# Performance work log

Hardware: AMD Instinct MI355X
Metric: run time of the kernel (lower is better)

The kernel has to match this reference:

```python
import jax, jax.numpy as jnp
import numpy as np

N = 100000        # nodes
E_RAND = 1600000  # random edges (avg degree 16)
D_IN = 64
D_OUT = 64


def setup_inputs() -> dict:
    key = jax.random.key(0)
    k1, k2, k3, k4, k5 = jax.random.split(key, 5)
    x = jax.random.normal(k1, (N, D_IN), dtype=jnp.float32)
    rows = jax.random.randint(k2, (E_RAND,), 0, N)
    cols = jax.random.randint(k3, (E_RAND,), 0, N)
    loops = jnp.arange(N)  # self loops appended at the end (matches remove+add_self_loops order)
    edge_index = jnp.stack([jnp.concatenate([rows, loops]),
                            jnp.concatenate([cols, loops])]).astype(jnp.int64)
    W = (jax.random.normal(k4, (D_IN, D_OUT), dtype=jnp.float32) / np.float32(np.sqrt(D_IN)))
    b = jax.random.normal(k5, (D_OUT,), dtype=jnp.float32) * 0.01
    return {"x": x, "edge_index": edge_index, "W": W, "b": b}


def reference(x, edge_index, W, b):
    row, col = edge_index[0], edge_index[1]
    # lin(x[row]) == (x @ W + b)[row]; transform once then gather (cheaper, same math)
    xl = x @ W + b                      # [N, D_OUT]
    x_i = xl[row]                       # [E, D_OUT] gather by destination
    x_j = xl[col]                       # [E, D_OUT] gather by source
    alpha = jnp.sum(x_i * x_j, axis=-1)  # [E] per-edge score
    alpha = jax.nn.leaky_relu(alpha, negative_slope=0.2)
    # segment-wise softmax over neighborhoods keyed by row
    m = jax.ops.segment_max(alpha, row, num_segments=N)
    m = jnp.where(jnp.isfinite(m), m, 0.0)   # isolated nodes -> -inf max, neutralize
    e = jnp.exp(alpha - m[row])
    s = jax.ops.segment_sum(e, row, num_segments=N)
    alpha = e / (s[row] + 1e-16)
    # dropout(p=0.6) skipped: reference runs in eval mode (deterministic)
    out = jax.ops.segment_sum(x_j * alpha[:, None], row, num_segments=N)  # [N, D_OUT]
    return out
```

## Files before the change

### kernel.cpp

```cpp
#include <hip/hip_runtime.h>
#include <hip/hip_bf16.h>


#define LEAKY_SLOPE 0.2f
#define BK_SHIFT 6
#define BK_NODES 64
#define CAP 1408
#define NBMAX 2048
#define CH 8192

typedef __attribute__((ext_vector_type(8))) short short8;
typedef __attribute__((ext_vector_type(4))) float f32x4;

struct HiLo { short hi, lo; };

__device__ __forceinline__ HiLo split2(float f) {
    HiLo r;
    unsigned u = __float_as_uint(f);
    r.hi = (short)(u >> 16);
    float fh = __uint_as_float(u & 0xFFFF0000u);
    r.lo = (short)(__float_as_uint(f - fh) >> 16);
    return r;
}

__device__ __forceinline__ float bfbits2f(unsigned short u) {
    return __uint_as_float(((unsigned)u) << 16);
}

__global__ __launch_bounds__(256) void k_linear(const float* __restrict__ x,
                                                const float* __restrict__ W,
                                                const float* __restrict__ b,
                                                float* __restrict__ xl,
                                                unsigned short* __restrict__ xlh,
                                                int* __restrict__ cursor,
                                                int ncur, int N, int ntiles) {
    __shared__ __align__(16) short Wt_hi[64 * 72];
    __shared__ __align__(16) short Wt_lo[64 * 72];

    int tid = threadIdx.x;
    int gid = blockIdx.x * 256 + tid;
    if (gid < ncur) cursor[gid] = 0;

    for (int i = tid; i < 4096; i += 256) {
        int k = i >> 6, n = i & 63;
        HiLo h = split2(W[i]);
        Wt_hi[n * 72 + k] = h.hi;
        Wt_lo[n * 72 + k] = h.lo;
    }
    __syncthreads();

    int wave = tid >> 6, lane = tid & 63;
    int tile = blockIdx.x * 4 + wave;
    if (tile >= ntiles) return;
    int node0 = tile * 16;

    int m = lane & 15;
    int quad = lane >> 4;

    f32x4 acc[4] = {{0.f, 0.f, 0.f, 0.f}, {0.f, 0.f, 0.f, 0.f},
                    {0.f, 0.f, 0.f, 0.f}, {0.f, 0.f, 0.f, 0.f}};

#pragma unroll
    for (int ks = 0; ks < 64; ks += 32) {
        const float* xr = x + (size_t)(node0 + m) * 64 + ks + quad * 8;
        float4 xa = *(const float4*)xr;
        float4 xb = *(const float4*)(xr + 4);
        short8 a_hi, a_lo;
        {
            HiLo h0 = split2(xa.x), h1 = split2(xa.y), h2 = split2(xa.z), h3 = split2(xa.w);
            HiLo h4 = split2(xb.x), h5 = split2(xb.y), h6 = split2(xb.z), h7 = split2(xb.w);
            a_hi[0] = h0.hi; a_lo[0] = h0.lo;  a_hi[1] = h1.hi; a_lo[1] = h1.lo;
            a_hi[2] = h2.hi; a_lo[2] = h2.lo;  a_hi[3] = h3.hi; a_lo[3] = h3.lo;
            a_hi[4] = h4.hi; a_lo[4] = h4.lo;  a_hi[5] = h5.hi; a_lo[5] = h5.lo;
            a_hi[6] = h6.hi; a_lo[6] = h6.lo;  a_hi[7] = h7.hi; a_lo[7] = h7.lo;
        }

#pragma unroll
        for (int g = 0; g < 4; ++g) {
            int n = g * 16 + m;
            int off = n * 72 + ks + quad * 8;
            short8 bh = *(const short8*)&Wt_hi[off];
            short8 bl = *(const short8*)&Wt_lo[off];
            acc[g] = __builtin_amdgcn_mfma_f32_16x16x32_bf16(a_hi, bh, acc[g], 0, 0, 0);
            acc[g] = __builtin_amdgcn_mfma_f32_16x16x32_bf16(a_lo, bh, acc[g], 0, 0, 0);
            acc[g] = __builtin_amdgcn_mfma_f32_16x16x32_bf16(a_hi, bl, acc[g], 0, 0, 0);
        }
    }

#pragma unroll
    for (int g = 0; g < 4; ++g) {
        float bias = b[g * 16 + m];
#pragma unroll
        for (int r = 0; r < 4; ++r) {
            int node = node0 + quad * 4 + r;
            if (node < N) {
                float v = acc[g][r] + bias;
                xl[(size_t)node * 64 + g * 16 + m] = v;
                xlh[(size_t)node * 64 + g * 16 + m] =
                    (unsigned short)(__float_as_uint(v) >> 16);
            }
        }
    }
}

__global__ __launch_bounds__(1024) void k_msplit(const int* __restrict__ row,
                                                 const int* __restrict__ col,
                                                 int* __restrict__ cursor,
                                                 unsigned* __restrict__ staging,
                                                 int E, int NB) {
    __shared__ int cnt[NBMAX], base[NBMAX], pos[NBMAX];
    int tid = threadIdx.x;
    int e0 = blockIdx.x * CH;
    int e1 = min(E, e0 + CH);

    for (int i = tid; i < NB; i += 1024) { cnt[i] = 0; pos[i] = 0; }
    __syncthreads();
    for (int e = e0 + tid; e < e1; e += 1024)
        atomicAdd(&cnt[row[e] >> BK_SHIFT], 1);
    __syncthreads();
    for (int i = tid; i < NB; i += 1024)
        base[i] = cnt[i] ? atomicAdd(&cursor[i * 16], cnt[i]) : 0;
    __syncthreads();
    for (int e = e0 + tid; e < e1; e += 1024) {
        int r = row[e], c = col[e];
        int bkt = r >> BK_SHIFT;
        int p = base[bkt] + atomicAdd(&pos[bkt], 1);
        if (p < CAP)
            staging[(size_t)bkt * CAP + p] =
                ((unsigned)(r & (BK_NODES - 1)) << 17) | (unsigned)c;
    }
}

__device__ __forceinline__ float red16(float d) {
    d += __shfl_xor(d, 1, 64);
    d += __shfl_xor(d, 2, 64);
    d += __shfl_xor(d, 4, 64);
    d += __shfl_xor(d, 8, 64);
    return d;
}

__device__ __forceinline__ void upd(float& m, float& l, float4& acc,
                                    float a, float4 xj) {
    if (a <= m) {
        float p = __expf(a - m);
        l += p;
        acc.x += p * xj.x; acc.y += p * xj.y;
        acc.z += p * xj.z; acc.w += p * xj.w;
    } else {
        float sc = __expf(m - a);
        l = l * sc + 1.0f;
        acc.x = acc.x * sc + xj.x; acc.y = acc.y * sc + xj.y;
        acc.z = acc.z * sc + xj.z; acc.w = acc.w * sc + xj.w;
        m = a;
    }
}

__device__ __forceinline__ float4 ld_bf4(const unsigned short* p) {
    ushort4 u = *(const ushort4*)p;
    float4 f;
    f.x = bfbits2f(u.x); f.y = bfbits2f(u.y);
    f.z = bfbits2f(u.z); f.w = bfbits2f(u.w);
    return f;
}

__global__ __launch_bounds__(256) void k_sortfused(const float* __restrict__ xl,
                                                   const unsigned short* __restrict__ xlh,
                                                   const unsigned* __restrict__ staging,
                                                   const int* __restrict__ cursor,
                                                   float* __restrict__ out, int N) {
    __shared__ int colsh[CAP];
    __shared__ int deg[BK_NODES], sc[BK_NODES], cur[BK_NODES];

    int bkt = blockIdx.x;
    int tid = threadIdx.x;
    int cnt = min(cursor[bkt * 16], CAP);
    const unsigned* st = staging + (size_t)bkt * CAP;

    if (tid < BK_NODES) { deg[tid] = 0; cur[tid] = 0; }
    __syncthreads();

    for (int e = tid; e < cnt; e += 256) atomicAdd(&deg[st[e] >> 17], 1);
    __syncthreads();

    if (tid < BK_NODES) sc[tid] = deg[tid];
    __syncthreads();
#pragma unroll
    for (int o = 1; o < BK_NODES; o <<= 1) {
        int v = 0;
        if (tid < BK_NODES && tid >= o) v = sc[tid - o];
        __syncthreads();
        if (tid < BK_NODES) sc[tid] += v;
        __syncthreads();
    }

    for (int e = tid; e < cnt; e += 256) {
        unsigned pk = st[e];
        int rl = pk >> 17;
        int p = sc[rl] - deg[rl] + atomicAdd(&cur[rl], 1);
        colsh[p] = (int)(pk & 0x1FFFFu);
    }
    __syncthreads();

    int grp = tid >> 4;
    int g = tid & 15;
    for (int n0 = grp; n0 < BK_NODES; n0 += 16) {
        int node = bkt * BK_NODES + n0;
        if (node >= N) continue;
        int beg = sc[n0] - deg[n0];
        int end = sc[n0];
        float4 xi = ((const float4*)xl)[(size_t)node * 16 + g];

        float m = -INFINITY, l = 0.0f;
        float4 acc = {0.f, 0.f, 0.f, 0.f};

        int e = beg;
        for (; e + 4 <= end; e += 4) {
            int c0 = colsh[e], c1 = colsh[e + 1], c2 = colsh[e + 2], c3 = colsh[e + 3];
            float4 xj0 = ld_bf4(xlh + (size_t)c0 * 64 + 4 * g);
            float4 xj1 = ld_bf4(xlh + (size_t)c1 * 64 + 4 * g);
            float4 xj2 = ld_bf4(xlh + (size_t)c2 * 64 + 4 * g);
            float4 xj3 = ld_bf4(xlh + (size_t)c3 * 64 + 4 * g);
            float d0 = red16(xi.x * xj0.x + xi.y * xj0.y + xi.z * xj0.z + xi.w * xj0.w);
            float d1 = red16(xi.x * xj1.x + xi.y * xj1.y + xi.z * xj1.z + xi.w * xj1.w);
            float d2 = red16(xi.x * xj2.x + xi.y * xj2.y + xi.z * xj2.z + xi.w * xj2.w);
            float d3 = red16(xi.x * xj3.x + xi.y * xj3.y + xi.z * xj3.z + xi.w * xj3.w);
            upd(m, l, acc, (d0 >= 0.f) ? d0 : LEAKY_SLOPE * d0, xj0);
            upd(m, l, acc, (d1 >= 0.f) ? d1 : LEAKY_SLOPE * d1, xj1);
            upd(m, l, acc, (d2 >= 0.f) ? d2 : LEAKY_SLOPE * d2, xj2);
            upd(m, l, acc, (d3 >= 0.f) ? d3 : LEAKY_SLOPE * d3, xj3);
        }
        for (; e < end; ++e) {
            int c = colsh[e];
            float4 xj = ld_bf4(xlh + (size_t)c * 64 + 4 * g);
            float d = red16(xi.x * xj.x + xi.y * xj.y + xi.z * xj.z + xi.w * xj.w);
            upd(m, l, acc, (d >= 0.f) ? d : LEAKY_SLOPE * d, xj);
        }
        float inv = 1.0f / (l + 1e-16f);
        float4 o = {acc.x * inv, acc.y * inv, acc.z * inv, acc.w * inv};
        ((float4*)out)[(size_t)node * 16 + g] = o;
    }
}

extern "C" void kernel_launch(void* const* d_in, const int* in_sizes, int n_in,
                              void* d_out, int out_size, void* d_ws, size_t ws_size,
                              hipStream_t stream) {
    const float* x = (const float*)d_in[0];
    const int* ei = (const int*)d_in[1];
    const float* W = (const float*)d_in[2];
    const float* b = (const float*)d_in[3];

    const int N = in_sizes[0] / 64;
    const int E = in_sizes[1] / 2;
    const int NO = N * 64;
    const int NB = (N + BK_NODES - 1) >> BK_SHIFT;
    const int* row = ei;
    const int* col = ei + E;

    float* out = (float*)d_out;

    float* ws = (float*)d_ws;
    float* xl           = ws;
    unsigned short* xlh = (unsigned short*)(xl + (size_t)NO);
    int* cursor         = (int*)(xlh + (size_t)NO);
    unsigned* staging   = (unsigned*)(cursor + NB * 16);

    const int ntiles = (N + 15) / 16;
    const int lblocks = (ntiles + 3) / 4;
    k_linear<<<lblocks, 256, 0, stream>>>(x, W, b, xl, xlh, cursor, NB * 16, N, ntiles);
    k_msplit<<<(E + CH - 1) / CH, 1024, 0, stream>>>(row, col, cursor, staging, E, NB);
    k_sortfused<<<NB, 256, 0, stream>>>(xl, xlh, staging, cursor, out, N);
}
```

Measured before the change: 184.5 us.

## Merge linear and bucket-split into one launch with per-chunk offset tables

Fuses the linear-transform kernel and the edge bucketing kernel into a single launch whose blocks branch on block index, sharing LDS through a union. Global atomics on per-bucket cursors are replaced by per-chunk local prefix scans that write chunk-major staging plus an offset table. The aggregation kernel then rebuilds each bucket's edge list by scanning the per-chunk lengths and binary-searching chunks. This removes one launch and the global atomic contention and cursor zeroing, at the cost of scattered gathers from many chunks in the consumer, 256-thread split blocks instead of 1024, and a 128-chunk limit.

```diff
diff --git a/kernel.cpp b/kernel.cpp
--- a/kernel.cpp
+++ b/kernel.cpp
@@ -6,8 +6,9 @@
 #define BK_SHIFT 6
 #define BK_NODES 64
 #define CAP 1408
-#define NBMAX 2048
-#define CH 8192
+#define NBMAX 1600
+#define CH 16384
+#define NCH_MAX 128
 
 typedef __attribute__((ext_vector_type(8))) short short8;
 typedef __attribute__((ext_vector_type(4))) float f32x4;
@@ -27,107 +28,124 @@
     return __uint_as_float(((unsigned)u) << 16);
 }
 
-__global__ __launch_bounds__(256) void k_linear(const float* __restrict__ x,
-                                                const float* __restrict__ W,
-                                                const float* __restrict__ b,
-                                                float* __restrict__ xl,
-                                                unsigned short* __restrict__ xlh,
-                                                int* __restrict__ cursor,
-                                                int ncur, int N, int ntiles) {
-    __shared__ __align__(16) short Wt_hi[64 * 72];
-    __shared__ __align__(16) short Wt_lo[64 * 72];
-
+union PreShMem {
+    struct { short wt_hi[64 * 72]; short wt_lo[64 * 72]; } lin;
+    struct { int cnt[NBMAX], scn[NBMAX], pos[NBMAX], segsum[256]; } ms;
+};
+
+__global__ __launch_bounds__(256) void k_pre(const float* __restrict__ x,
+                                             const float* __restrict__ W,
+                                             const float* __restrict__ b,
+                                             const int* __restrict__ row,
+                                             const int* __restrict__ col,
+                                             float* __restrict__ xl,
+                                             unsigned short* __restrict__ xlh,
+                                             int* __restrict__ ofs,
+                                             unsigned* __restrict__ staging,
+                                             int N, int E, int NB,
+                                             int ntiles, int lblocks) {
+    __shared__ PreShMem sh;
     int tid = threadIdx.x;
-    int gid = blockIdx.x * 256 + tid;
-    if (gid < ncur) cursor[gid] = 0;
-
-    for (int i = tid; i < 4096; i += 256) {
-        int k = i >> 6, n = i & 63;
-        HiLo h = split2(W[i]);
-        Wt_hi[n * 72 + k] = h.hi;
-        Wt_lo[n * 72 + k] = h.lo;
-    }
-    __syncthreads();
-
-    int wave = tid >> 6, lane = tid & 63;
-    int tile = blockIdx.x * 4 + wave;
-    if (tile >= ntiles) return;
-    int node0 = tile * 16;
-
-    int m = lane & 15;
-    int quad = lane >> 4;
-
-    f32x4 acc[4] = {{0.f, 0.f, 0.f, 0.f}, {0.f, 0.f, 0.f, 0.f},
-                    {0.f, 0.f, 0.f, 0.f}, {0.f, 0.f, 0.f, 0.f}};
-
-#pragma unroll
-    for (int ks = 0; ks < 64; ks += 32) {
-        const float* xr = x + (size_t)(node0 + m) * 64 + ks + quad * 8;
-        float4 xa = *(const float4*)xr;
-        float4 xb = *(const float4*)(xr + 4);
-        short8 a_hi, a_lo;
-        {
-            HiLo h0 = split2(xa.x), h1 = split2(xa.y), h2 = split2(xa.z), h3 = split2(xa.w);
-            HiLo h4 = split2(xb.x), h5 = split2(xb.y), h6 = split2(xb.z), h7 = split2(xb.w);
-            a_hi[0] = h0.hi; a_lo[0] = h0.lo;  a_hi[1] = h1.hi; a_lo[1] = h1.lo;
-            a_hi[2] = h2.hi; a_lo[2] = h2.lo;  a_hi[3] = h3.hi; a_lo[3] = h3.lo;
-            a_hi[4] = h4.hi; a_lo[4] = h4.lo;  a_hi[5] = h5.hi; a_lo[5] = h5.lo;
-            a_hi[6] = h6.hi; a_lo[6] = h6.lo;  a_hi[7] = h7.hi; a_lo[7] = h7.lo;
+
+    if ((int)blockIdx.x < lblocks) {
+        for (int i = tid; i < 4096; i += 256) {
+            int k = i >> 6, n = i & 63;
+            HiLo h = split2(W[i]);
+            sh.lin.wt_hi[n * 72 + k] = h.hi;
+            sh.lin.wt_lo[n * 72 + k] = h.lo;
+        }
+        __syncthreads();
+
+        int wave = tid >> 6, lane = tid & 63;
+        int tile = blockIdx.x * 4 + wave;
+        if (tile >= ntiles) return;
+        int node0 = tile * 16;
+        int m = lane & 15;
+        int quad = lane >> 4;
+
+        f32x4 acc[4] = {{0.f, 0.f, 0.f, 0.f}, {0.f, 0.f, 0.f, 0.f},
+                        {0.f, 0.f, 0.f, 0.f}, {0.f, 0.f, 0.f, 0.f}};
+
+#pragma unroll
+        for (int ks = 0; ks < 64; ks += 32) {
+            const float* xr = x + (size_t)(node0 + m) * 64 + ks + quad * 8;
+            float4 xa = *(const float4*)xr;
+            float4 xb = *(const float4*)(xr + 4);
+            short8 a_hi, a_lo;
+            {
+                HiLo h0 = split2(xa.x), h1 = split2(xa.y), h2 = split2(xa.z), h3 = split2(xa.w);
+                HiLo h4 = split2(xb.x), h5 = split2(xb.y), h6 = split2(xb.z), h7 = split2(xb.w);
+                a_hi[0] = h0.hi; a_lo[0] = h0.lo;  a_hi[1] = h1.hi; a_lo[1] = h1.lo;
+                a_hi[2] = h2.hi; a_lo[2] = h2.lo;  a_hi[3] = h3.hi; a_lo[3] = h3.lo;
+                a_hi[4] = h4.hi; a_lo[4] = h4.lo;  a_hi[5] = h5.hi; a_lo[5] = h5.lo;
+                a_hi[6] = h6.hi; a_lo[6] = h6.lo;  a_hi[7] = h7.hi; a_lo[7] = h7.lo;
+            }
+#pragma unroll
+            for (int g = 0; g < 4; ++g) {
+                int n = g * 16 + m;
+                int off = n * 72 + ks + quad * 8;
+                short8 bh = *(const short8*)&sh.lin.wt_hi[off];
+                short8 bl = *(const short8*)&sh.lin.wt_lo[off];
+                acc[g] = __builtin_amdgcn_mfma_f32_16x16x32_bf16(a_hi, bh, acc[g], 0, 0, 0);
+                acc[g] = __builtin_amdgcn_mfma_f32_16x16x32_bf16(a_lo, bh, acc[g], 0, 0, 0);
+                acc[g] = __builtin_amdgcn_mfma_f32_16x16x32_bf16(a_hi, bl, acc[g], 0, 0, 0);
+            }
         }
 
 #pragma unroll
         for (int g = 0; g < 4; ++g) {
-            int n = g * 16 + m;
-            int off = n * 72 + ks + quad * 8;
-            short8 bh = *(const short8*)&Wt_hi[off];
-            short8 bl = *(const short8*)&Wt_lo[off];
-            acc[g] = __builtin_amdgcn_mfma_f32_16x16x32_bf16(a_hi, bh, acc[g], 0, 0, 0);
-            acc[g] = __builtin_amdgcn_mfma_f32_16x16x32_bf16(a_lo, bh, acc[g], 0, 0, 0);
-            acc[g] = __builtin_amdgcn_mfma_f32_16x16x32_bf16(a_hi, bl, acc[g], 0, 0, 0);
-        }
-    }
-
-#pragma unroll
-    for (int g = 0; g < 4; ++g) {
-        float bias = b[g * 16 + m];
-#pragma unroll
-        for (int r = 0; r < 4; ++r) {
-            int node = node0 + quad * 4 + r;
-            if (node < N) {
-                float v = acc[g][r] + bias;
-                xl[(size_t)node * 64 + g * 16 + m] = v;
-                xlh[(size_t)node * 64 + g * 16 + m] =
-                    (unsigned short)(__float_as_uint(v) >> 16);
+            float bias = b[g * 16 + m];
+#pragma unroll
+            for (int r = 0; r < 4; ++r) {
+                int node = node0 + quad * 4 + r;
+                if (node < N) {
+                    float v = acc[g][r] + bias;
+                    xl[(size_t)node * 64 + g * 16 + m] = v;
+                    xlh[(size_t)node * 64 + g * 16 + m] =
+                        (unsigned short)(__float_as_uint(v) >> 16);
+                }
             }
         }
-    }
-}
-
-__global__ __launch_bounds__(1024) void k_msplit(const int* __restrict__ row,
-                                                 const int* __restrict__ col,
-                                                 int* __restrict__ cursor,
-                                                 unsigned* __restrict__ staging,
-                                                 int E, int NB) {
-    __shared__ int cnt[NBMAX], base[NBMAX], pos[NBMAX];
-    int tid = threadIdx.x;
-    int e0 = blockIdx.x * CH;
-    int e1 = min(E, e0 + CH);
-
-    for (int i = tid; i < NB; i += 1024) { cnt[i] = 0; pos[i] = 0; }
-    __syncthreads();
-    for (int e = e0 + tid; e < e1; e += 1024)
-        atomicAdd(&cnt[row[e] >> BK_SHIFT], 1);
-    __syncthreads();
-    for (int i = tid; i < NB; i += 1024)
-        base[i] = cnt[i] ? atomicAdd(&cursor[i * 16], cnt[i]) : 0;
-    __syncthreads();
-    for (int e = e0 + tid; e < e1; e += 1024) {
-        int r = row[e], c = col[e];
-        int bkt = r >> BK_SHIFT;
-        int p = base[bkt] + atomicAdd(&pos[bkt], 1);
-        if (p < CAP)
-            staging[(size_t)bkt * CAP + p] =
-                ((unsigned)(r & (BK_NODES - 1)) << 17) | (unsigned)c;
+    } else {
+        int vbk = (int)blockIdx.x - lblocks;
+        int e0 = vbk * CH;
+        int e1 = min(E, e0 + CH);
+
+        for (int i = tid; i < NB; i += 256) { sh.ms.cnt[i] = 0; sh.ms.pos[i] = 0; }
+        __syncthreads();
+
+        for (int e = e0 + tid; e < e1; e += 256)
+            atomicAdd(&sh.ms.cnt[row[e] >> BK_SHIFT], 1);
+        __syncthreads();
+
+        const int SEG = (NBMAX + 255) / 256;
+        int segbeg = tid * SEG;
+        int segend = min(NB, segbeg + SEG);
+        int s = 0;
+        for (int i = segbeg; i < segend; ++i) { int v = sh.ms.cnt[i]; sh.ms.scn[i] = s; s += v; }
+        sh.ms.segsum[tid] = s;
+        __syncthreads();
+        for (int o = 1; o < 256; o <<= 1) {
+            int v = (tid >= o) ? sh.ms.segsum[tid - o] : 0;
+            __syncthreads();
+            sh.ms.segsum[tid] += v;
+            __syncthreads();
+        }
+        int segoff = (tid == 0) ? 0 : sh.ms.segsum[tid - 1];
+        for (int i = segbeg; i < segend; ++i) sh.ms.scn[i] += segoff;
+        __syncthreads();
+
+        int* orow = ofs + (size_t)vbk * (NB + 1);
+        for (int i = tid; i < NB; i += 256) orow[i] = sh.ms.scn[i];
+        if (tid == 0) orow[NB] = e1 - e0;
+
+        unsigned* stg = staging + (size_t)vbk * CH;
+        for (int e = e0 + tid; e < e1; e += 256) {
+            int r = row[e], c = col[e];
+            int bkt = r >> BK_SHIFT;
+            int p = sh.ms.scn[bkt] + atomicAdd(&sh.ms.pos[bkt], 1);
+            stg[p] = ((unsigned)(r & (BK_NODES - 1)) << 17) | (unsigned)c;
+        }
     }
 }
 
@@ -163,23 +181,62 @@
     return f;
 }
 
+__device__ __forceinline__ float dot4(float4 a, float4 b) {
+    return a.x * b.x + a.y * b.y + a.z * b.z + a.w * b.w;
+}
+
 __global__ __launch_bounds__(256) void k_sortfused(const float* __restrict__ xl,
                                                    const unsigned short* __restrict__ xlh,
                                                    const unsigned* __restrict__ staging,
-                                                   const int* __restrict__ cursor,
-                                                   float* __restrict__ out, int N) {
+                                                   const int* __restrict__ ofs,
+                                                   float* __restrict__ out,
+                                                   int N, int NB, int nch) {
+    __shared__ int raw[CAP];
     __shared__ int colsh[CAP];
     __shared__ int deg[BK_NODES], sc[BK_NODES], cur[BK_NODES];
+    __shared__ int lenarr[NCH_MAX];
+    __shared__ int chbeg[NCH_MAX + 1];
+    __shared__ int chofs[NCH_MAX];
 
     int bkt = blockIdx.x;
     int tid = threadIdx.x;
-    int cnt = min(cursor[bkt * 16], CAP);
-    const unsigned* st = staging + (size_t)bkt * CAP;
+
+    if (tid < NCH_MAX) {
+        int len = 0;
+        if (tid < nch) {
+            const int* orow = ofs + (size_t)tid * (NB + 1);
+            int o0 = orow[bkt], o1 = orow[bkt + 1];
+            chofs[tid] = o0;
+            len = o1 - o0;
+        }
+        lenarr[tid] = len;
+    }
+    __syncthreads();
+    for (int o = 1; o < NCH_MAX; o <<= 1) {
+        int v = 0;
+        if (tid < NCH_MAX && tid >= o) v = lenarr[tid - o];
+        __syncthreads();
+        if (tid < NCH_MAX) lenarr[tid] += v;
+        __syncthreads();
+    }
+    if (tid <= nch) chbeg[tid] = (tid == 0) ? 0 : lenarr[tid - 1];
+    __syncthreads();
+
+    int cnt = min(chbeg[nch], CAP);
+
+    for (int i = tid; i < cnt; i += 256) {
+        int lo = 0, hi = nch - 1;
+        while (lo < hi) {
+            int mid = (lo + hi + 1) >> 1;
+            if (chbeg[mid] <= i) lo = mid; else hi = mid - 1;
+        }
+        raw[i] = (int)staging[(size_t)lo * CH + chofs[lo] + (i - chbeg[lo])];
+    }
 
     if (tid < BK_NODES) { deg[tid] = 0; cur[tid] = 0; }
     __syncthreads();
 
-    for (int e = tid; e < cnt; e += 256) atomicAdd(&deg[st[e] >> 17], 1);
+    for (int e = tid; e < cnt; e += 256) atomicAdd(&deg[((unsigned)raw[e]) >> 17], 1);
     __syncthreads();
 
     if (tid < BK_NODES) sc[tid] = deg[tid];
@@ -194,7 +251,7 @@
     }
 
     for (int e = tid; e < cnt; e += 256) {
-        unsigned pk = st[e];
+        unsigned pk = (unsigned)raw[e];
         int rl = pk >> 17;
         int p = sc[rl] - deg[rl] + atomicAdd(&cur[rl], 1);
         colsh[p] = (int)(pk & 0x1FFFFu);
@@ -220,10 +277,10 @@
             float4 xj1 = ld_bf4(xlh + (size_t)c1 * 64 + 4 * g);
             float4 xj2 = ld_bf4(xlh + (size_t)c2 * 64 + 4 * g);
             float4 xj3 = ld_bf4(xlh + (size_t)c3 * 64 + 4 * g);
-            float d0 = red16(xi.x * xj0.x + xi.y * xj0.y + xi.z * xj0.z + xi.w * xj0.w);
-            float d1 = red16(xi.x * xj1.x + xi.y * xj1.y + xi.z * xj1.z + xi.w * xj1.w);
-            float d2 = red16(xi.x * xj2.x + xi.y * xj2.y + xi.z * xj2.z + xi.w * xj2.w);
-            float d3 = red16(xi.x * xj3.x + xi.y * xj3.y + xi.z * xj3.z + xi.w * xj3.w);
+            float d0 = red16(dot4(xi, xj0));
+            float d1 = red16(dot4(xi, xj1));
+            float d2 = red16(dot4(xi, xj2));
+            float d3 = red16(dot4(xi, xj3));
             upd(m, l, acc, (d0 >= 0.f) ? d0 : LEAKY_SLOPE * d0, xj0);
             upd(m, l, acc, (d1 >= 0.f) ? d1 : LEAKY_SLOPE * d1, xj1);
             upd(m, l, acc, (d2 >= 0.f) ? d2 : LEAKY_SLOPE * d2, xj2);
@@ -232,7 +289,7 @@
         for (; e < end; ++e) {
             int c = colsh[e];
             float4 xj = ld_bf4(xlh + (size_t)c * 64 + 4 * g);
-            float d = red16(xi.x * xj.x + xi.y * xj.y + xi.z * xj.z + xi.w * xj.w);
+            float d = red16(dot4(xi, xj));
             upd(m, l, acc, (d >= 0.f) ? d : LEAKY_SLOPE * d, xj);
         }
         float inv = 1.0f / (l + 1e-16f);
@@ -253,6 +310,7 @@
     const int E = in_sizes[1] / 2;
     const int NO = N * 64;
     const int NB = (N + BK_NODES - 1) >> BK_SHIFT;
+    const int NCH = (E + CH - 1) / CH;
     const int* row = ei;
     const int* col = ei + E;
 
@@ -261,12 +319,13 @@
     float* ws = (float*)d_ws;
     float* xl           = ws;
     unsigned short* xlh = (unsigned short*)(xl + (size_t)NO);
-    int* cursor         = (int*)(xlh + (size_t)NO);
-    unsigned* staging   = (unsigned*)(cursor + NB * 16);
+    int* ofs            = (int*)(xlh + (size_t)NO);
+    unsigned* staging   = (unsigned*)(ofs + (size_t)NCH * (NB + 1));
 
     const int ntiles = (N + 15) / 16;
     const int lblocks = (ntiles + 3) / 4;
-    k_linear<<<lblocks, 256, 0, stream>>>(x, W, b, xl, xlh, cursor, NB * 16, N, ntiles);
-    k_msplit<<<(E + CH - 1) / CH, 1024, 0, stream>>>(row, col, cursor, staging, E, NB);
-    k_sortfused<<<NB, 256, 0, stream>>>(xl, xlh, staging, cursor, out, N);
-}
+
+    k_pre<<<lblocks + NCH, 256, 0, stream>>>(x, W, b, row, col, xl, xlh,
+                                             ofs, staging, N, E, NB, ntiles, lblocks);
+    k_sortfused<<<NB, 256, 0, stream>>>(xl, xlh, staging, ofs, out, N, NB, NCH);
+}
```

Result: slower. 188.6 us (+2.2%).
